# Performance work log

Measured on AMD Instinct MI355X. Metric: run time of the kernel, lower is better.

The kernel has to match this reference:

```python
import jax, jax.numpy as jnp
import numpy as np

N = 50000          # num nodes
E = 800000         # num edges (avg degree 16)
R = 8              # num relations
IN = 128
H0 = 256
H1 = 64


def _w(key, shape, fan_in):
    return jax.random.normal(key, shape, dtype=jnp.float32) * (1.0 / np.sqrt(fan_in))


def setup_inputs() -> dict:
    key = jax.random.key(0)
    ks = jax.random.split(key, 16)
    x = jax.random.normal(ks[0], (N, IN), dtype=jnp.float32)
    edge_index = jax.random.randint(ks[1], (2, E), 0, N, dtype=jnp.int64)
    edge_type = jax.random.randint(ks[2], (E,), 0, R, dtype=jnp.int64)
    return {
        "x": x,
        "edge_index": edge_index,
        "edge_type": edge_type,
        # RGCNConv params: per-relation weights [R, in, out], root weight [in, out], bias [out]
        "W1": _w(ks[3], (R, IN, H0), IN), "root1": _w(ks[4], (IN, H0), IN), "b1": jnp.zeros((H0,), jnp.float32),
        "W2": _w(ks[5], (R, H0, H0), H0), "root2": _w(ks[6], (H0, H0), H0), "b2": jnp.zeros((H0,), jnp.float32),
        "W3": _w(ks[7], (R, H0, H0), H0), "root3": _w(ks[8], (H0, H0), H0), "b3": jnp.zeros((H0,), jnp.float32),
        "W4": _w(ks[9], (R, H0, H1), H0), "root4": _w(ks[10], (H0, H1), H0), "b4": jnp.zeros((H1,), jnp.float32),
    }


def rgcn_layer(x, edge_index, edge_type, W, root, bias):
    """PyG RGCNConv: out_i = x_i @ root + sum_r (1/|N_r(i)|) sum_{j in N_r(i)} x_j @ W_r + bias.
    Aggregation is linear, so aggregate source features per (relation, dst) first,
    then apply the R small GEMMs — avoids per-edge [E, out] message materialization."""
    src, dst = edge_index[0], edge_index[1]
    seg = edge_type * N + dst                      # combined (relation, dst) segment id
    nseg = R * N
    agg = jax.ops.segment_sum(x[src], seg, num_segments=nseg)          # [R*N, in]
    cnt = jax.ops.segment_sum(jnp.ones((seg.shape[0],), x.dtype), seg, num_segments=nseg)
    agg = agg / jnp.maximum(cnt, 1.0)[:, None]                          # mean per (r, i)
    agg = agg.reshape(R, N, x.shape[1])                                 # [R, N, in]
    return jnp.einsum('rni,rio->no', agg, W) + x @ root + bias


def reference(x, edge_index, edge_type, W1, root1, b1, W2, root2, b2, W3, root3, b3, W4, root4, b4):
    h = jax.nn.relu(rgcn_layer(x, edge_index, edge_type, W1, root1, b1))
    h = jax.nn.relu(rgcn_layer(h, edge_index, edge_type, W2, root2, b2))
    h = jax.nn.relu(rgcn_layer(h, edge_index, edge_type, W3, root3, b3))
    return rgcn_layer(h, edge_index, edge_type, W4, root4, b4)
```

## Files before the change

kernel.cpp:

```cpp
#include <hip/hip_runtime.h>

#define N_NODES 50000
#define N_PAD   50048
#define N_EDGES 800000
#define N_REL   8
#define NSEG    (N_REL * N_NODES)
#define NSEG_PAD 400384
#define SCAN_NB 391
#define NSTRIPE 391
#define NSTRIPE64 782
#define SPX     49
#define SPX64   98

typedef short bf16x8 __attribute__((ext_vector_type(8)));
typedef float f32x4  __attribute__((ext_vector_type(4)));

__device__ __forceinline__ ushort f2bf(float f) {
    union { float f; unsigned u; } c; c.f = f;
    unsigned u = c.u + 0x7fffu + ((c.u >> 16) & 1u);
    return (ushort)(u >> 16);
}
__device__ __forceinline__ void add8(float* s, uint4 v) {
    unsigned u[4] = {v.x, v.y, v.z, v.w};
    #pragma unroll
    for (int k = 0; k < 4; ++k) {
        s[2 * k]     += __uint_as_float(u[k] << 16);
        s[2 * k + 1] += __uint_as_float(u[k] & 0xffff0000u);
    }
}
__device__ __forceinline__ void fma8(float* s, uint4 v, float w) {
    unsigned u[4] = {v.x, v.y, v.z, v.w};
    #pragma unroll
    for (int k = 0; k < 4; ++k) {
        s[2 * k]     = fmaf(__uint_as_float(u[k] << 16),        w, s[2 * k]);
        s[2 * k + 1] = fmaf(__uint_as_float(u[k] & 0xffff0000u), w, s[2 * k + 1]);
    }
}
__device__ __forceinline__ void async16(const ushort* g, ushort* l) {
    __builtin_amdgcn_global_load_lds((const __attribute__((address_space(1))) void*)g,
                                     (__attribute__((address_space(3))) void*)l, 16, 0, 0);
}


__global__ void count_edges(const int* __restrict__ dst, const int* __restrict__ et,
                            int* __restrict__ cnt) {
    int e = blockIdx.x * 256 + threadIdx.x;
    if (e < N_EDGES) atomicAdd(&cnt[dst[e] * N_REL + et[e]], 1);
}

__global__ __launch_bounds__(256) void scan_pass1(const int* __restrict__ cnt,
                                                  int* __restrict__ sums) {
    __shared__ int sc[256];
    int b = blockIdx.x, t = threadIdx.x;
    int base = b * 1024 + t * 4;
    int v = 0;
    #pragma unroll
    for (int i = 0; i < 4; ++i) { int idx = base + i; if (idx < NSEG) v += cnt[idx]; }
    sc[t] = v; __syncthreads();
    for (int off = 1; off < 256; off <<= 1) {
        int x = (t >= off) ? sc[t - off] : 0;
        __syncthreads(); sc[t] += x; __syncthreads();
    }
    if (t == 255) sums[b] = sc[255];
}

__global__ __launch_bounds__(512) void scan_pass2(int* __restrict__ sums, int nb) {
    __shared__ int sc[512];
    int t = threadIdx.x;
    int v = (t < nb) ? sums[t] : 0;
    sc[t] = v; __syncthreads();
    for (int off = 1; off < 512; off <<= 1) {
        int x = (t >= off) ? sc[t - off] : 0;
        __syncthreads(); sc[t] += x; __syncthreads();
    }
    if (t < nb) sums[t] = sc[t] - v;
}

__global__ __launch_bounds__(256) void scan_pass3(const int* __restrict__ cnt,
                                                  const int* __restrict__ sums,
                                                  int* __restrict__ row_ptr) {
    __shared__ int sc[256];
    int b = blockIdx.x, t = threadIdx.x;
    int base = b * 1024 + t * 4;
    int e[4]; int v = 0;
    #pragma unroll
    for (int i = 0; i < 4; ++i) { int idx = base + i; e[i] = (idx < NSEG) ? cnt[idx] : 0; v += e[i]; }
    sc[t] = v; __syncthreads();
    for (int off = 1; off < 256; off <<= 1) {
        int x = (t >= off) ? sc[t - off] : 0;
        __syncthreads(); sc[t] += x; __syncthreads();
    }
    int run = sums[b] + (sc[t] - v);
    #pragma unroll
    for (int i = 0; i < 4; ++i) {
        int idx = base + i;
        if (idx < NSEG) row_ptr[idx] = run;
        run += e[i];
    }
    if (b == 0 && t == 0) row_ptr[NSEG] = N_EDGES;
}

__global__ void place_edges(const int* __restrict__ src, const int* __restrict__ dst,
                            const int* __restrict__ et, const int* __restrict__ row_ptr,
                            int* __restrict__ cnt, int* __restrict__ sorted) {
    int e = blockIdx.x * 256 + threadIdx.x;
    if (e >= N_EDGES) return;
    int r = et[e];
    int key = dst[e] * N_REL + r;
    int old = atomicSub(&cnt[key], 1);
    int r0 = row_ptr[key];
    int c = row_ptr[key + 1] - r0;
    sorted[r0 + old - 1] = src[e] | (r << 17) | (c << 20);
}

__global__ void convert_weights(const float* __restrict__ W, const float* __restrict__ root,
                                ushort* __restrict__ BT, int K, int O, int NPAD) {
    int idx = blockIdx.x * 256 + threadIdx.x;
    if (idx >= NPAD * K) return;
    int col = idx / K, i = idx % K;
    float v = 0.0f;
    if (col < N_REL * O) {
        int r = col / O, o = col % O;
        v = W[((size_t)r * K + i) * O + o];
    } else if (col < (N_REL + 1) * O) {
        v = root[(size_t)i * O + (col - N_REL * O)];
    }
    BT[idx] = f2bf(v);
}

__global__ void convert_weights2(const float* __restrict__ W, const float* __restrict__ root,
                                 ushort* __restrict__ BT, int K, int O) {
    int idx = blockIdx.x * 256 + threadIdx.x;
    if (idx >= O * 9 * K) return;
    int o = idx / (9 * K), k = idx % (9 * K);
    float v;
    if (k < 8 * K) { int r = k / K, i = k % K; v = W[((size_t)r * K + i) * O + o]; }
    else v = root[(size_t)(k - 8 * K) * O + o];
    BT[idx] = f2bf(v);
}

__global__ void f32_to_bf16(const float* __restrict__ in, ushort* __restrict__ out, int n4) {
    int i = blockIdx.x * 256 + threadIdx.x;
    if (i >= n4) return;
    float4 v = ((const float4*)in)[i];
    ushort4 s; s.x = f2bf(v.x); s.y = f2bf(v.y); s.z = f2bf(v.z); s.w = f2bf(v.w);
    ((ushort4*)out)[i] = s;
}

template<int K>
__global__ __launch_bounds__(256)
void agg_gather(const ushort* __restrict__ X, const int* __restrict__ row_ptr,
                const int* __restrict__ sorted, ushort* __restrict__ AGG) {
    constexpr int TPN = K / 8;
    constexpr int SPB = 256 / TPN;
    const int seg = blockIdx.x * SPB + threadIdx.x / TPN;
    const int c0 = (threadIdx.x % TPN) * 8;
    const int p0 = row_ptr[seg], p1 = row_ptr[seg + 1];
    float sum[8] = {};
    const ushort* Xc = X + c0;
    int e = p0;
    for (; e + 4 <= p1; e += 4) {
        int s0 = sorted[e] & 0x1FFFF, s1 = sorted[e + 1] & 0x1FFFF;
        int s2 = sorted[e + 2] & 0x1FFFF, s3 = sorted[e + 3] & 0x1FFFF;
        uint4 v0 = *(const uint4*)(Xc + (size_t)s0 * K);
        uint4 v1 = *(const uint4*)(Xc + (size_t)s1 * K);
        uint4 v2 = *(const uint4*)(Xc + (size_t)s2 * K);
        uint4 v3 = *(const uint4*)(Xc + (size_t)s3 * K);
        add8(sum, v0); add8(sum, v1); add8(sum, v2); add8(sum, v3);
    }
    for (; e < p1; ++e)
        add8(sum, *(const uint4*)(Xc + (size_t)(sorted[e] & 0x1FFFF) * K));
    ushort o[8];
    if (p1 > p0) {
        float inv = 1.0f / (float)(p1 - p0);
        #pragma unroll
        for (int k = 0; k < 8; ++k) o[k] = f2bf(sum[k] * inv);
    } else {
        #pragma unroll
        for (int k = 0; k < 8; ++k) o[k] = 0;
    }
    *(uint4*)(AGG + (size_t)seg * K + c0) = *(const uint4*)o;
}

template<int K>
__global__ __launch_bounds__(256)
void rgcn_gemm(const ushort* __restrict__ AGG, const ushort* __restrict__ X,
               const ushort* __restrict__ BT, const float* __restrict__ bias,
               ushort* __restrict__ H) {
    constexpr int KTOT  = 9 * K;
    constexpr int NK1   = K / 4;
    constexpr int NSTEP = NK1 + K / 32;

    const int f = blockIdx.x;
    const int g = f & 7, m = f >> 3;
    const int y = g + 8 * (m >> 1);
    const int ct = m & 1;
    if (y >= NSTRIPE64) return;
    const int row0 = y * 64;
    const int col0 = ct * 128;

    __shared__ ushort SMEM[12288];
    const int t = threadIdx.x, lane = t & 63, w = t >> 6;
    const int l16 = lane & 15, q = lane >> 4;
    const int wm = (w & 1) * 32;
    const int wn = (w >> 1) * 64;
    const int qx = (q ^ ((l16 >> 1) & 3)) * 8;

    const int cA = w * 64 + lane;
    const int rA = cA >> 2;
    const int jA = (cA & 3) ^ ((rA >> 1) & 3);
    const size_t gaA = (size_t)rA * (8 * K) + (size_t)jA * 8;
    const size_t gaX = (size_t)rA * K + (size_t)jA * 8;
    const int cB1 = cA + 256;
    const int rB1 = cB1 >> 2;
    const int jB1 = (cB1 & 3) ^ ((rB1 >> 1) & 3);
    const size_t gb0 = (size_t)rA * KTOT + (size_t)jA * 8;
    const size_t gb1 = (size_t)rB1 * KTOT + (size_t)jB1 * 8;

    const ushort* Abase = AGG + (size_t)row0 * (8 * K);
    const ushort* Xbase = X + (size_t)row0 * K;
    const ushort* Bbase = BT + (size_t)col0 * KTOT;

    auto STAGE = [&](int b, int s) {
        ushort* As = SMEM + b * 6144;
        ushort* Bs = As + 2048;
        if (s < NK1) async16(Abase + (size_t)s * 32 + gaA, &As[w * 512]);
        else         async16(Xbase + (size_t)(s - NK1) * 32 + gaX, &As[w * 512]);
        const ushort* pb = Bbase + (size_t)s * 32;
        async16(pb + gb0, &Bs[w * 512]);
        async16(pb + gb1, &Bs[(w + 4) * 512]);
    };

    f32x4 acc[2][4] = {};
    auto COMPUTE = [&](int b) {
        ushort* As = SMEM + b * 6144;
        ushort* Bs = As + 2048;
        bf16x8 a[2], bb[4];
        #pragma unroll
        for (int i = 0; i < 2; ++i)
            a[i] = *(const bf16x8*)&As[(wm + i * 16 + l16) * 32 + qx];
        #pragma unroll
        for (int j = 0; j < 4; ++j)
            bb[j] = *(const bf16x8*)&Bs[(wn + j * 16 + l16) * 32 + qx];
        #pragma unroll
        for (int i = 0; i < 2; ++i)
            #pragma unroll
            for (int j = 0; j < 4; ++j)
                acc[i][j] = __builtin_amdgcn_mfma_f32_16x16x32_bf16(a[i], bb[j], acc[i][j], 0, 0, 0);
    };

    STAGE(0, 0);
    __syncthreads();
    for (int s = 0; s < NSTEP; s += 2) {
        STAGE(1, s + 1);
        COMPUTE(0);
        __syncthreads();
        if (s + 2 < NSTEP) STAGE(0, s + 2);
        COMPUTE(1);
        __syncthreads();
    }

    float bj[4];
    #pragma unroll
    for (int j = 0; j < 4; ++j) bj[j] = bias[col0 + wn + j * 16 + l16];
    ushort* Ts = &SMEM[w * 2304];
    const int rr2 = lane >> 3, cc = (lane & 7) * 8;
    #pragma unroll
    for (int i = 0; i < 2; ++i)
        #pragma unroll
        for (int j = 0; j < 4; ++j)
            #pragma unroll
            for (int r = 0; r < 4; ++r) {
                float v = fmaxf(acc[i][j][r] + bj[j], 0.0f);
                Ts[(i * 16 + q * 4 + r) * 72 + j * 16 + l16] = f2bf(v);
            }
    #pragma unroll
    for (int p = 0; p < 4; ++p) {
        int row = p * 8 + rr2;
        uint4 v = *(const uint4*)&Ts[row * 72 + cc];
        *(uint4*)(H + (size_t)(row0 + wm + row) * 256 + col0 + wn + cc) = v;
    }
}

template<int K, int CTS, int NW>
__global__ __launch_bounds__(256)
void gemm_mfma(const ushort* __restrict__ A, const ushort* __restrict__ BT,
               ushort* __restrict__ Y) {
    const int f = blockIdx.x;
    const int g = f & 7, m = f >> 3;
    const int y = g + 8 * (m / CTS);
    const int ct = m % CTS;
    if (y >= NSTRIPE) return;
    const int row0 = y * 128;
    const int col0 = ct * 128;

    __shared__ ushort SMEM[16384];
    const int t = threadIdx.x;
    const int lane = t & 63;
    const int w = t >> 6;
    const int l16 = lane & 15, q = lane >> 4;
    const int wm = (w & 1) * 64, wn = (w >> 1) * 64;

    const int c0i = w * 64 + lane;
    const int c1i = c0i + 256;
    const int r0i = c0i >> 2, r1i = c1i >> 2;
    const int j0i = (c0i & 3) ^ ((r0i >> 1) & 3);
    const int j1i = (c1i & 3) ^ ((r1i >> 1) & 3);
    const size_t ga0 = (size_t)r0i * K + (size_t)j0i * 8;
    const size_t ga1 = (size_t)r1i * K + (size_t)j1i * 8;
    const ushort* Ab = A + (size_t)row0 * K;
    const ushort* Bb = BT + (size_t)col0 * K;

    const int qx = (q ^ ((l16 >> 1) & 3)) * 8;

    f32x4 acc[4][4] = {};

    auto STAGE = [&](int b, int k0) {
        ushort* As = SMEM + b * 8192;
        ushort* Bs = As + 4096;
        async16(Ab + k0 + ga0, &As[w * 512]);
        async16(Ab + k0 + ga1, &As[(w + 4) * 512]);
        async16(Bb + k0 + ga0, &Bs[w * 512]);
        async16(Bb + k0 + ga1, &Bs[(w + 4) * 512]);
    };
    auto COMPUTE = [&](int b) {
        ushort* As = SMEM + b * 8192;
        ushort* Bs = As + 4096;
        bf16x8 a[4], bb[4];
        #pragma unroll
        for (int i = 0; i < 4; ++i) {
            a[i]  = *(const bf16x8*)&As[(wm + i * 16 + l16) * 32 + qx];
            bb[i] = *(const bf16x8*)&Bs[(wn + i * 16 + l16) * 32 + qx];
        }
        #pragma unroll
        for (int i = 0; i < 4; ++i)
            #pragma unroll
            for (int j = 0; j < 4; ++j)
                acc[i][j] = __builtin_amdgcn_mfma_f32_16x16x32_bf16(a[i], bb[j], acc[i][j], 0, 0, 0);
    };

    constexpr int NSTEP = K / 32;
    STAGE(0, 0);
    __syncthreads();
    #pragma unroll
    for (int s = 0; s < NSTEP; ++s) {
        if (s + 1 < NSTEP) STAGE((s + 1) & 1, 32 * (s + 1));
        COMPUTE(s & 1);
        __syncthreads();
    }

    ushort* Ts = &SMEM[w * 32 * 72];
    const int rr = lane >> 3;
    const int cc = (lane & 7) * 8;
    #pragma unroll
    for (int half = 0; half < 2; ++half) {
        #pragma unroll
        for (int i = 0; i < 2; ++i)
            #pragma unroll
            for (int j = 0; j < 4; ++j)
                #pragma unroll
                for (int r = 0; r < 4; ++r)
                    Ts[(i * 16 + q * 4 + r) * 72 + j * 16 + l16] = f2bf(acc[half * 2 + i][j][r]);
        #pragma unroll
        for (int p = 0; p < 4; ++p) {
            int row = p * 8 + rr;
            uint4 v = *(const uint4*)&Ts[row * 72 + cc];
            *(uint4*)(Y + (size_t)(row0 + wm + half * 32 + row) * NW + col0 + wn + cc) = v;
        }
    }
}

template<int O>
__global__ __launch_bounds__(256)
void gather_kernel(const ushort* __restrict__ Y, int NW,
                   const int* __restrict__ row_ptr, const int* __restrict__ sorted,
                   const float* __restrict__ bias,
                   float* __restrict__ out_f32, ushort* __restrict__ out_bf16, int relu) {
    constexpr int TPN = O / 8;
    int d = blockIdx.x * (256 / TPN) + threadIdx.x / TPN;
    if (d >= N_NODES) return;
    int c0 = (threadIdx.x % TPN) * 8;
    int p0 = row_ptr[d * N_REL];
    int p1 = row_ptr[d * N_REL + N_REL];
    float sum[8] = {};
    add8(sum, *(const uint4*)(Y + (size_t)d * NW + N_REL * O + c0));
    #pragma unroll
    for (int k = 0; k < 8; ++k) sum[k] += bias[c0 + k];
    const ushort* Yc = Y + c0;
    #define EDGE_LD(sx) (*(const uint4*)(Yc + (size_t)((sx) & 0x1FFFF) * NW + ((((sx) >> 17) & 7) * O)))
    #define EDGE_W(sx)  (1.0f / (float)((unsigned)(sx) >> 20))
    int e = p0;
    for (; e + 4 <= p1; e += 4) {
        int s0 = sorted[e], s1 = sorted[e + 1], s2 = sorted[e + 2], s3 = sorted[e + 3];
        uint4 v0 = EDGE_LD(s0);
        uint4 v1 = EDGE_LD(s1);
        uint4 v2 = EDGE_LD(s2);
        uint4 v3 = EDGE_LD(s3);
        fma8(sum, v0, EDGE_W(s0));
        fma8(sum, v1, EDGE_W(s1));
        fma8(sum, v2, EDGE_W(s2));
        fma8(sum, v3, EDGE_W(s3));
    }
    for (; e < p1; ++e) {
        int s = sorted[e];
        uint4 v = EDGE_LD(s);
        fma8(sum, v, EDGE_W(s));
    }
    #undef EDGE_LD
    #undef EDGE_W
    if (relu) {
        #pragma unroll
        for (int k = 0; k < 8; ++k) sum[k] = fmaxf(sum[k], 0.0f);
    }
    if (out_bf16) {
        ushort o[8];
        #pragma unroll
        for (int k = 0; k < 8; ++k) o[k] = f2bf(sum[k]);
        *(uint4*)(out_bf16 + (size_t)d * O + c0) = *(const uint4*)o;
    } else {
        float* p = out_f32 + (size_t)d * O + c0;
        *(float4*)p = make_float4(sum[0], sum[1], sum[2], sum[3]);
        *(float4*)(p + 4) = make_float4(sum[4], sum[5], sum[6], sum[7]);
    }
}


extern "C" void kernel_launch(void* const* d_in, const int* in_sizes, int n_in,
                              void* d_out, int out_size, void* d_ws, size_t ws_size,
                              hipStream_t stream) {
    const float* x  = (const float*)d_in[0];
    const int*   ei = (const int*)d_in[1];
    const int*   et = (const int*)d_in[2];
    const float* W[4]  = {(const float*)d_in[3], (const float*)d_in[6], (const float*)d_in[9],  (const float*)d_in[12]};
    const float* RT[4] = {(const float*)d_in[4], (const float*)d_in[7], (const float*)d_in[10], (const float*)d_in[13]};
    const float* BI[4] = {(const float*)d_in[5], (const float*)d_in[8], (const float*)d_in[11], (const float*)d_in[14]};
    const int* src = ei;
    const int* dst = ei + N_EDGES;

    char* ws = (char*)d_ws;
    size_t off = 0;
    auto take = [&](size_t bytes) -> char* {
        char* p = ws + off;
        off = (off + bytes + 255) & ~(size_t)255;
        return p;
    };
    int* row_ptr = (int*)take((size_t)(NSEG + 1) * 4);
    int* sorted  = (int*)take((size_t)N_EDGES * 4);
    ushort* BT1 = (ushort*)take((size_t)256 * 1152 * 2);
    ushort* BT2 = (ushort*)take((size_t)256 * 2304 * 2);
    ushort* BT3 = (ushort*)take((size_t)256 * 2304 * 2);
    ushort* BT4 = (ushort*)take((size_t)640 * 256 * 2);
    ushort* Ha  = (ushort*)take((size_t)N_PAD * 256 * 2);
    ushort* Hb  = (ushort*)take((size_t)N_PAD * 256 * 2);
    ushort* AGG = (ushort*)take((size_t)NSEG_PAD * 256 * 2);
    int*    cnt  = (int*)AGG;
    int*    sums = (int*)((char*)AGG + (size_t)(NSEG + 64) * 4);
    ushort* X0   = (ushort*)((char*)AGG + 104000000);
    ushort* Y640 = AGG;

    hipMemsetAsync(cnt, 0, (size_t)NSEG * 4, stream);
    count_edges<<<(N_EDGES + 255) / 256, 256, 0, stream>>>(dst, et, cnt);
    scan_pass1<<<SCAN_NB, 256, 0, stream>>>(cnt, sums);
    scan_pass2<<<1, 512, 0, stream>>>(sums, SCAN_NB);
    scan_pass3<<<SCAN_NB, 256, 0, stream>>>(cnt, sums, row_ptr);
    place_edges<<<(N_EDGES + 255) / 256, 256, 0, stream>>>(src, dst, et, row_ptr, cnt, sorted);

    convert_weights2<<<(256 * 1152 + 255) / 256, 256, 0, stream>>>(W[0], RT[0], BT1, 128, 256);
    convert_weights2<<<(256 * 2304 + 255) / 256, 256, 0, stream>>>(W[1], RT[1], BT2, 256, 256);
    convert_weights2<<<(256 * 2304 + 255) / 256, 256, 0, stream>>>(W[2], RT[2], BT3, 256, 256);
    convert_weights<<<(640 * 256 + 255) / 256, 256, 0, stream>>>(W[3], RT[3], BT4, 256, 64, 640);

    f32_to_bf16<<<(N_NODES * 128 / 4 + 255) / 256, 256, 0, stream>>>(x, X0, N_NODES * 128 / 4);

    const int GG = 8 * SPX64 * 2;
    agg_gather<128><<<NSEG / 16, 256, 0, stream>>>(X0, row_ptr, sorted, AGG);
    rgcn_gemm<128><<<GG, 256, 0, stream>>>(AGG, X0, BT1, BI[0], Ha);

    agg_gather<256><<<NSEG / 8, 256, 0, stream>>>(Ha, row_ptr, sorted, AGG);
    rgcn_gemm<256><<<GG, 256, 0, stream>>>(AGG, Ha, BT2, BI[1], Hb);

    agg_gather<256><<<NSEG / 8, 256, 0, stream>>>(Hb, row_ptr, sorted, AGG);
    rgcn_gemm<256><<<GG, 256, 0, stream>>>(AGG, Hb, BT3, BI[2], Ha);

    const int G5 = 8 * SPX * 5;
    gemm_mfma<256, 5, 640><<<G5, 256, 0, stream>>>(Ha, BT4, Y640);
    gather_kernel<64><<<dim3((N_NODES + 31) / 32), 256, 0, stream>>>(
        Y640, 640, row_ptr, sorted, BI[3], (float*)d_out, nullptr, 0);
}
```

Measured before the change: 732.9 us.

## Enlarge rgcn_gemm tile to 128 rows with triple-buffered async pipeline

The fused RGCN GEMM tile grows from 64x128 to 128x128, so each wave computes a 64x64 sub-tile and each B load is reused across twice as many rows. The loop becomes a three-stage LDS ring with explicit vmcnt waits plus barriers in place of full __syncthreads, and MFMA issue gets a raised s_setprio. The aim is less B-operand traffic per output and better overlap of loads with compute. The cost is double the LDS and more accumulator registers, which can cut occupancy, and fewer blocks on a GPU with many CUs.

```diff
diff --git a/kernel.cpp b/kernel.cpp
--- a/kernel.cpp
+++ b/kernel.cpp
@@ -8,9 +8,7 @@
 #define NSEG_PAD 400384
 #define SCAN_NB 391
 #define NSTRIPE 391
-#define NSTRIPE64 782
 #define SPX     49
-#define SPX64   98
 
 typedef short bf16x8 __attribute__((ext_vector_type(8)));
 typedef float f32x4  __attribute__((ext_vector_type(4)));
@@ -40,6 +38,8 @@
     __builtin_amdgcn_global_load_lds((const __attribute__((address_space(1))) void*)g,
                                      (__attribute__((address_space(3))) void*)l, 16, 0, 0);
 }
+
+#define WAITBAR(N) asm volatile("s_waitcnt vmcnt(" #N ")\ns_barrier" ::: "memory")
 
 
 __global__ void count_edges(const int* __restrict__ dst, const int* __restrict__ et,
@@ -189,96 +189,112 @@
                ushort* __restrict__ H) {
     constexpr int KTOT  = 9 * K;
     constexpr int NK1   = K / 4;
-    constexpr int NSTEP = NK1 + K / 32;
+    constexpr int NSTEP = KTOT / 32;
 
     const int f = blockIdx.x;
     const int g = f & 7, m = f >> 3;
     const int y = g + 8 * (m >> 1);
     const int ct = m & 1;
-    if (y >= NSTRIPE64) return;
-    const int row0 = y * 64;
+    if (y >= NSTRIPE) return;
+    const int row0 = y * 128;
     const int col0 = ct * 128;
 
-    __shared__ ushort SMEM[12288];
+    __shared__ ushort SMEM[24576];
     const int t = threadIdx.x, lane = t & 63, w = t >> 6;
     const int l16 = lane & 15, q = lane >> 4;
-    const int wm = (w & 1) * 32;
-    const int wn = (w >> 1) * 64;
+    const int wm = (w & 1) * 64, wn = (w >> 1) * 64;
     const int qx = (q ^ ((l16 >> 1) & 3)) * 8;
 
-    const int cA = w * 64 + lane;
-    const int rA = cA >> 2;
-    const int jA = (cA & 3) ^ ((rA >> 1) & 3);
-    const size_t gaA = (size_t)rA * (8 * K) + (size_t)jA * 8;
-    const size_t gaX = (size_t)rA * K + (size_t)jA * 8;
-    const int cB1 = cA + 256;
-    const int rB1 = cB1 >> 2;
-    const int jB1 = (cB1 & 3) ^ ((rB1 >> 1) & 3);
-    const size_t gb0 = (size_t)rA * KTOT + (size_t)jA * 8;
-    const size_t gb1 = (size_t)rB1 * KTOT + (size_t)jB1 * 8;
-
+    const int c0i = w * 64 + lane, c1i = c0i + 256;
+    const int r0i = c0i >> 2, r1i = c1i >> 2;
+    const int j0i = (c0i & 3) ^ ((r0i >> 1) & 3);
+    const int j1i = (c1i & 3) ^ ((r1i >> 1) & 3);
+    const size_t gaA0 = (size_t)r0i * (8 * K) + (size_t)j0i * 8;
+    const size_t gaA1 = (size_t)r1i * (8 * K) + (size_t)j1i * 8;
+    const size_t gaX0 = (size_t)r0i * K + (size_t)j0i * 8;
+    const size_t gaX1 = (size_t)r1i * K + (size_t)j1i * 8;
+    const size_t gb0  = (size_t)r0i * KTOT + (size_t)j0i * 8;
+    const size_t gb1  = (size_t)r1i * KTOT + (size_t)j1i * 8;
     const ushort* Abase = AGG + (size_t)row0 * (8 * K);
     const ushort* Xbase = X + (size_t)row0 * K;
     const ushort* Bbase = BT + (size_t)col0 * KTOT;
 
     auto STAGE = [&](int b, int s) {
-        ushort* As = SMEM + b * 6144;
-        ushort* Bs = As + 2048;
-        if (s < NK1) async16(Abase + (size_t)s * 32 + gaA, &As[w * 512]);
-        else         async16(Xbase + (size_t)(s - NK1) * 32 + gaX, &As[w * 512]);
+        ushort* As = SMEM + b * 8192;
+        ushort* Bs = As + 4096;
+        if (s < NK1) {
+            const ushort* pa = Abase + (size_t)s * 32;
+            async16(pa + gaA0, &As[w * 512]);
+            async16(pa + gaA1, &As[(w + 4) * 512]);
+        } else {
+            const ushort* pa = Xbase + (size_t)(s - NK1) * 32;
+            async16(pa + gaX0, &As[w * 512]);
+            async16(pa + gaX1, &As[(w + 4) * 512]);
+        }
         const ushort* pb = Bbase + (size_t)s * 32;
         async16(pb + gb0, &Bs[w * 512]);
         async16(pb + gb1, &Bs[(w + 4) * 512]);
     };
 
-    f32x4 acc[2][4] = {};
+    f32x4 acc[4][4] = {};
     auto COMPUTE = [&](int b) {
-        ushort* As = SMEM + b * 6144;
-        ushort* Bs = As + 2048;
-        bf16x8 a[2], bb[4];
-        #pragma unroll
-        for (int i = 0; i < 2; ++i)
-            a[i] = *(const bf16x8*)&As[(wm + i * 16 + l16) * 32 + qx];
-        #pragma unroll
-        for (int j = 0; j < 4; ++j)
-            bb[j] = *(const bf16x8*)&Bs[(wn + j * 16 + l16) * 32 + qx];
+        ushort* As = SMEM + b * 8192;
+        ushort* Bs = As + 4096;
+        bf16x8 a[4], bb[4];
+        #pragma unroll
+        for (int i = 0; i < 4; ++i) {
+            a[i]  = *(const bf16x8*)&As[(wm + i * 16 + l16) * 32 + qx];
+            bb[i] = *(const bf16x8*)&Bs[(wn + i * 16 + l16) * 32 + qx];
+        }
+        __builtin_amdgcn_s_setprio(1);
+        #pragma unroll
+        for (int i = 0; i < 4; ++i)
+            #pragma unroll
+            for (int j = 0; j < 4; ++j)
+                acc[i][j] = __builtin_amdgcn_mfma_f32_16x16x32_bf16(a[i], bb[j], acc[i][j], 0, 0, 0);
+        __builtin_amdgcn_s_setprio(0);
+    };
+
+    STAGE(0, 0);
+    STAGE(1, 1);
+    int b = 0;
+    for (int s = 0; s < NSTEP; ++s) {
+        if (s + 2 < NSTEP) {
+            int b2 = b + 2; if (b2 >= 3) b2 -= 3;
+            STAGE(b2, s + 2);
+            WAITBAR(8);
+        } else if (s + 1 < NSTEP) {
+            WAITBAR(4);
+        } else {
+            WAITBAR(0);
+        }
+        COMPUTE(b);
+        __builtin_amdgcn_s_barrier();
+        ++b; if (b == 3) b = 0;
+    }
+
+    float bj[4];
+    #pragma unroll
+    for (int j = 0; j < 4; ++j) bj[j] = bias[col0 + wn + j * 16 + l16];
+    ushort* Ts = &SMEM[w * 2304];
+    const int rr2 = lane >> 3, cc2 = (lane & 7) * 8;
+    #pragma unroll
+    for (int half = 0; half < 2; ++half) {
         #pragma unroll
         for (int i = 0; i < 2; ++i)
             #pragma unroll
             for (int j = 0; j < 4; ++j)
-                acc[i][j] = __builtin_amdgcn_mfma_f32_16x16x32_bf16(a[i], bb[j], acc[i][j], 0, 0, 0);
-    };
-
-    STAGE(0, 0);
-    __syncthreads();
-    for (int s = 0; s < NSTEP; s += 2) {
-        STAGE(1, s + 1);
-        COMPUTE(0);
-        __syncthreads();
-        if (s + 2 < NSTEP) STAGE(0, s + 2);
-        COMPUTE(1);
-        __syncthreads();
-    }
-
-    float bj[4];
-    #pragma unroll
-    for (int j = 0; j < 4; ++j) bj[j] = bias[col0 + wn + j * 16 + l16];
-    ushort* Ts = &SMEM[w * 2304];
-    const int rr2 = lane >> 3, cc = (lane & 7) * 8;
-    #pragma unroll
-    for (int i = 0; i < 2; ++i)
-        #pragma unroll
-        for (int j = 0; j < 4; ++j)
-            #pragma unroll
-            for (int r = 0; r < 4; ++r) {
-                float v = fmaxf(acc[i][j][r] + bj[j], 0.0f);
-                Ts[(i * 16 + q * 4 + r) * 72 + j * 16 + l16] = f2bf(v);
-            }
-    #pragma unroll
-    for (int p = 0; p < 4; ++p) {
-        int row = p * 8 + rr2;
-        uint4 v = *(const uint4*)&Ts[row * 72 + cc];
-        *(uint4*)(H + (size_t)(row0 + wm + row) * 256 + col0 + wn + cc) = v;
+                #pragma unroll
+                for (int r = 0; r < 4; ++r) {
+                    float v = fmaxf(acc[half * 2 + i][j][r] + bj[j], 0.0f);
+                    Ts[(i * 16 + q * 4 + r) * 72 + j * 16 + l16] = f2bf(v);
+                }
+        #pragma unroll
+        for (int p = 0; p < 4; ++p) {
+            int row = p * 8 + rr2;
+            uint4 v = *(const uint4*)&Ts[row * 72 + cc2];
+            *(uint4*)(H + (size_t)(row0 + wm + half * 32 + row) * 256 + col0 + wn + cc2) = v;
+        }
     }
 }
 
@@ -472,7 +488,7 @@
 
     f32_to_bf16<<<(N_NODES * 128 / 4 + 255) / 256, 256, 0, stream>>>(x, X0, N_NODES * 128 / 4);
 
-    const int GG = 8 * SPX64 * 2;
+    const int GG = 8 * SPX * 2;
     agg_gather<128><<<NSEG / 16, 256, 0, stream>>>(X0, row_ptr, sorted, AGG);
     rgcn_gemm<128><<<GG, 256, 0, stream>>>(AGG, X0, BT1, BI[0], Ha);
 
```

After: 701.0 us. 1.05x faster.

## Triple-buffer rgcn_gemm LDS pipeline with vmcnt-based waits and MFMA priority

Applied to the files above, without the earlier changes.

Replaces the double-buffered loop in rgcn_gemm with a three-stage LDS ring. Global-to-LDS loads run two steps ahead, and each step waits with an explicit s_waitcnt vmcnt plus s_barrier instead of a full __syncthreads that drains all loads. It also raises wave priority around the MFMA block. The goal is to hide global load latency better, at the cost of more shared memory per block, which may lower occupancy.

```diff
diff --git a/kernel.cpp b/kernel.cpp
--- a/kernel.cpp
+++ b/kernel.cpp
@@ -40,6 +40,8 @@
     __builtin_amdgcn_global_load_lds((const __attribute__((address_space(1))) void*)g,
                                      (__attribute__((address_space(3))) void*)l, 16, 0, 0);
 }
+
+#define WAITBAR(N) asm volatile("s_waitcnt vmcnt(" #N ")\ns_barrier" ::: "memory")
 
 
 __global__ void count_edges(const int* __restrict__ dst, const int* __restrict__ et,
@@ -189,7 +191,7 @@
                ushort* __restrict__ H) {
     constexpr int KTOT  = 9 * K;
     constexpr int NK1   = K / 4;
-    constexpr int NSTEP = NK1 + K / 32;
+    constexpr int NSTEP = KTOT / 32;
 
     const int f = blockIdx.x;
     const int g = f & 7, m = f >> 3;
@@ -199,24 +201,21 @@
     const int row0 = y * 64;
     const int col0 = ct * 128;
 
-    __shared__ ushort SMEM[12288];
+    __shared__ ushort SMEM[18432];
     const int t = threadIdx.x, lane = t & 63, w = t >> 6;
     const int l16 = lane & 15, q = lane >> 4;
     const int wm = (w & 1) * 32;
     const int wn = (w >> 1) * 64;
     const int qx = (q ^ ((l16 >> 1) & 3)) * 8;
 
-    const int cA = w * 64 + lane;
-    const int rA = cA >> 2;
-    const int jA = (cA & 3) ^ ((rA >> 1) & 3);
+    const int rA = t >> 2;
+    const int jA = (t & 3) ^ ((rA >> 1) & 3);
     const size_t gaA = (size_t)rA * (8 * K) + (size_t)jA * 8;
     const size_t gaX = (size_t)rA * K + (size_t)jA * 8;
-    const int cB1 = cA + 256;
-    const int rB1 = cB1 >> 2;
+    const int cB1 = t + 256, rB1 = cB1 >> 2;
     const int jB1 = (cB1 & 3) ^ ((rB1 >> 1) & 3);
     const size_t gb0 = (size_t)rA * KTOT + (size_t)jA * 8;
     const size_t gb1 = (size_t)rB1 * KTOT + (size_t)jB1 * 8;
-
     const ushort* Abase = AGG + (size_t)row0 * (8 * K);
     const ushort* Xbase = X + (size_t)row0 * K;
     const ushort* Bbase = BT + (size_t)col0 * KTOT;
@@ -228,7 +227,7 @@
         else         async16(Xbase + (size_t)(s - NK1) * 32 + gaX, &As[w * 512]);
         const ushort* pb = Bbase + (size_t)s * 32;
         async16(pb + gb0, &Bs[w * 512]);
-        async16(pb + gb1, &Bs[(w + 4) * 512]);
+        async16(pb + gb1, &Bs[2048 + w * 512]);
     };
 
     f32x4 acc[2][4] = {};
@@ -242,29 +241,38 @@
         #pragma unroll
         for (int j = 0; j < 4; ++j)
             bb[j] = *(const bf16x8*)&Bs[(wn + j * 16 + l16) * 32 + qx];
+        __builtin_amdgcn_s_setprio(1);
         #pragma unroll
         for (int i = 0; i < 2; ++i)
             #pragma unroll
             for (int j = 0; j < 4; ++j)
                 acc[i][j] = __builtin_amdgcn_mfma_f32_16x16x32_bf16(a[i], bb[j], acc[i][j], 0, 0, 0);
+        __builtin_amdgcn_s_setprio(0);
     };
 
     STAGE(0, 0);
-    __syncthreads();
-    for (int s = 0; s < NSTEP; s += 2) {
-        STAGE(1, s + 1);
-        COMPUTE(0);
-        __syncthreads();
-        if (s + 2 < NSTEP) STAGE(0, s + 2);
-        COMPUTE(1);
-        __syncthreads();
+    STAGE(1, 1);
+    int b = 0;
+    for (int s = 0; s < NSTEP; ++s) {
+        if (s + 2 < NSTEP) {
+            int b2 = b + 2; if (b2 >= 3) b2 -= 3;
+            STAGE(b2, s + 2);
+            WAITBAR(6);
+        } else if (s + 1 < NSTEP) {
+            WAITBAR(3);
+        } else {
+            WAITBAR(0);
+        }
+        COMPUTE(b);
+        __builtin_amdgcn_s_barrier();
+        ++b; if (b == 3) b = 0;
     }
 
     float bj[4];
     #pragma unroll
     for (int j = 0; j < 4; ++j) bj[j] = bias[col0 + wn + j * 16 + l16];
     ushort* Ts = &SMEM[w * 2304];
-    const int rr2 = lane >> 3, cc = (lane & 7) * 8;
+    const int rr2 = lane >> 3, cc2 = (lane & 7) * 8;
     #pragma unroll
     for (int i = 0; i < 2; ++i)
         #pragma unroll
@@ -277,8 +285,8 @@
     #pragma unroll
     for (int p = 0; p < 4; ++p) {
         int row = p * 8 + rr2;
-        uint4 v = *(const uint4*)&Ts[row * 72 + cc];
-        *(uint4*)(H + (size_t)(row0 + wm + row) * 256 + col0 + wn + cc) = v;
+        uint4 v = *(const uint4*)&Ts[row * 72 + cc2];
+        *(uint4*)(H + (size_t)(row0 + wm + row) * 256 + col0 + wn + cc2) = v;
     }
 }
 
```

Measured after the change: 739.2 us. About the same (+0.9%).
